# Kernel optimization log

Hardware: AMD Instinct MI355X
Metric: run time of the kernel (lower is better)

The kernel has to match this reference:

```python
import jax, jax.numpy as jnp
import numpy as np

TAIL_BOUND = 3.0
MIN_BIN_WIDTH = 1e-3
MIN_BIN_HEIGHT = 1e-3
SEARCH_EPS = 1e-6


def setup_inputs() -> dict:
    key = jax.random.key(0)
    k1, k2, k3, k4, k5 = jax.random.split(key, 5)
    B, D, K = 8192, 256, 8
    return {
        "x": jax.random.normal(k1, (B, D), dtype=jnp.float32),
        "w_": jax.random.normal(k2, (B, D, K), dtype=jnp.float32),
        "h_": jax.random.normal(k3, (B, D, K), dtype=jnp.float32),
        "dl_": jax.random.normal(k4, (B, D, 1), dtype=jnp.float32),
        "dr_": jax.random.normal(k5, (B, D, 1), dtype=jnp.float32),
    }


def _cumknots(unnorm, min_bin):
    # softmax -> min-width floor -> cumsum with exact 0/1 endpoints
    num_bins = unnorm.shape[-1]
    w = jax.nn.softmax(unnorm, axis=-1)
    w = min_bin + (1.0 - min_bin * num_bins) * w
    cum = jnp.cumsum(w, axis=-1)
    cum = cum.at[..., -1].set(1.0)
    pad = [(0, 0)] * (cum.ndim - 1) + [(1, 0)]
    cum = jnp.pad(cum, pad)
    return w, cum


def reference(x, w_, h_, dl_, dr_):
    num_bins = w_.shape[-1]
    left = bottom = -TAIL_BOUND
    right = top = TAIL_BOUND

    inside = (x >= left) & (x <= right)

    # map to unit interval; clamp keeps masked-out lanes numerically safe
    t = jnp.clip((x - left) / (right - left), 0.0, 1.0)

    widths, cumwidths = _cumknots(w_, MIN_BIN_WIDTH)       # [B,D,K], [B,D,K+1]
    heights, cumheights = _cumknots(h_, MIN_BIN_HEIGHT)

    slopes = heights / widths                              # [B,D,K]
    min1 = jnp.minimum(jnp.abs(slopes[..., :-1]), jnp.abs(slopes[..., 1:]))
    min2 = 0.5 * (widths[..., 1:] * slopes[..., :-1] + widths[..., :-1] * slopes[..., 1:]) \
           / (widths[..., :-1] + widths[..., 1:])
    mins = jnp.minimum(min1, min2)                         # [B,D,K-1]

    d_left = jax.nn.sigmoid(dl_) * 3.0 * slopes[..., :1]
    d_right = jax.nn.sigmoid(dr_) * 3.0 * slopes[..., -1:]
    d_mid = mins * (jnp.sign(slopes[..., :-1]) + jnp.sign(slopes[..., 1:]))
    derivs = jnp.concatenate([d_left, d_mid, d_right], axis=-1)  # [B,D,K+1]

    a = (derivs[..., :-1] + derivs[..., 1:] - 2.0 * slopes) / widths ** 2
    b = (3.0 * slopes - 2.0 * derivs[..., :-1] - derivs[..., 1:]) / widths
    c = derivs[..., :-1]
    d = cumheights[..., :-1]

    # searchsorted: sum(t >= knots) - 1, with eps bump on the last knot
    knots = cumwidths.at[..., -1].add(SEARCH_EPS)
    bin_idx = jnp.sum((t[..., None] >= knots).astype(jnp.int32), axis=-1) - 1
    bin_idx = jnp.clip(bin_idx, 0, num_bins - 1)[..., None]  # [B,D,1]

    take = lambda arr: jnp.take_along_axis(arr, bin_idx, axis=-1)[..., 0]
    ia, ib, ic, id_ = take(a), take(b), take(c), take(d)
    lw = take(cumwidths)

    sx = t - lw
    out_s = ia * sx ** 3 + ib * sx ** 2 + ic * sx + id_
    lad_s = jnp.log(jnp.abs(3.0 * ia * sx ** 2 + 2.0 * ib * sx + ic))

    out_s = jnp.clip(out_s, 0.0, 1.0) * (top - bottom) + bottom
    lad_s = lad_s + jnp.log(top - bottom) - jnp.log(right - left)

    outputs = jnp.where(inside, out_s, x)          # identity tails
    logabsdet = jnp.where(inside, lad_s, 0.0)
    return outputs, logabsdet
```

## Files before the change

kernel.cpp:

```cpp
#include <hip/hip_runtime.h>
#include <math.h>


constexpr int K = 8;
constexpr float TAIL = 3.0f;
constexpr float MIN_BIN = 0.001f;
constexpr float SEARCH_EPS = 1e-6f;

__device__ __forceinline__ float rcpf(float v) {
    return __builtin_amdgcn_rcpf(v);
}

__device__ __forceinline__ float signf(float v) {
    return (v > 0.0f ? 1.0f : (v < 0.0f ? -1.0f : 0.0f));
}

__global__ __launch_bounds__(256) void cbs_kernel(
    const float* __restrict__ x_,
    const float* __restrict__ w_,
    const float* __restrict__ h_,
    const float* __restrict__ dl_,
    const float* __restrict__ dr_,
    float* __restrict__ out,
    float* __restrict__ lad,
    int n)
{
    int i = blockIdx.x * blockDim.x + threadIdx.x;
    if (i >= n) return;

    const float4* w4 = (const float4*)w_ + 2 * (size_t)i;
    const float4* h4 = (const float4*)h_ + 2 * (size_t)i;
    float4 wa = w4[0], wb = w4[1];
    float4 ha = h4[0], hb = h4[1];

    float wr[K] = {wa.x, wa.y, wa.z, wa.w, wb.x, wb.y, wb.z, wb.w};
    float hr[K] = {ha.x, ha.y, ha.z, ha.w, hb.x, hb.y, hb.z, hb.w};

    float xv  = x_[i];
    float dlv = dl_[i];
    float drv = dr_[i];

    float mw = wr[0];
    #pragma unroll
    for (int k = 1; k < K; k++) mw = fmaxf(mw, wr[k]);
    float sw = 0.0f;
    #pragma unroll
    for (int k = 0; k < K; k++) { wr[k] = __expf(wr[k] - mw); sw += wr[k]; }
    float inv_sw = rcpf(sw);
    #pragma unroll
    for (int k = 0; k < K; k++) wr[k] = MIN_BIN + (1.0f - MIN_BIN * K) * (wr[k] * inv_sw);

    float mh = hr[0];
    #pragma unroll
    for (int k = 1; k < K; k++) mh = fmaxf(mh, hr[k]);
    float sh = 0.0f;
    #pragma unroll
    for (int k = 0; k < K; k++) { hr[k] = __expf(hr[k] - mh); sh += hr[k]; }
    float inv_sh = rcpf(sh);
    #pragma unroll
    for (int k = 0; k < K; k++) hr[k] = MIN_BIN + (1.0f - MIN_BIN * K) * (hr[k] * inv_sh);

    float cw[K + 1]; cw[0] = 0.0f;
    #pragma unroll
    for (int k = 0; k < K; k++) cw[k + 1] = cw[k] + wr[k];
    float ch[K + 1]; ch[0] = 0.0f;
    #pragma unroll
    for (int k = 0; k < K; k++) ch[k + 1] = ch[k] + hr[k];

    float s[K];
    #pragma unroll
    for (int k = 0; k < K; k++) s[k] = hr[k] * rcpf(wr[k]);

    float dv[K + 1];
    dv[0] = rcpf(1.0f + __expf(-dlv)) * 3.0f * s[0];
    dv[K] = rcpf(1.0f + __expf(-drv)) * 3.0f * s[K - 1];
    #pragma unroll
    for (int k = 0; k < K - 1; k++) {
        float m1 = fminf(fabsf(s[k]), fabsf(s[k + 1]));
        float m2 = 0.5f * (wr[k + 1] * s[k] + wr[k] * s[k + 1]) * rcpf(wr[k] + wr[k + 1]);
        float mn = fminf(m1, m2);
        dv[k + 1] = mn * (signf(s[k]) + signf(s[k + 1]));
    }

    float t = (xv + TAIL) * (1.0f / (2.0f * TAIL));
    t = fminf(fmaxf(t, 0.0f), 1.0f);

    int bin = 0;
    #pragma unroll
    for (int j = 1; j < K; j++) bin += (t >= cw[j]) ? 1 : 0;
    bin += (t >= 1.0f + SEARCH_EPS) ? 1 : 0;
    if (bin > K - 1) bin = K - 1;

    float wk = wr[0], sk = s[0], d0 = dv[0], d1 = dv[1], lw = cw[0], dd = ch[0];
    #pragma unroll
    for (int k = 1; k < K; k++) {
        bool sel = (bin == k);
        wk = sel ? wr[k]     : wk;
        sk = sel ? s[k]      : sk;
        d0 = sel ? dv[k]     : d0;
        d1 = sel ? dv[k + 1] : d1;
        lw = sel ? cw[k]     : lw;
        dd = sel ? ch[k]     : dd;
    }

    float inv_wk = rcpf(wk);
    float ia = (d0 + d1 - 2.0f * sk) * inv_wk * inv_wk;
    float ib = (3.0f * sk - 2.0f * d0 - d1) * inv_wk;
    float ic = d0;

    float sx = t - lw;
    float out_s = ((ia * sx + ib) * sx + ic) * sx + dd;
    float der   = (3.0f * ia * sx + 2.0f * ib) * sx + ic;
    float lad_s = __logf(fabsf(der));

    out_s = fminf(fmaxf(out_s, 0.0f), 1.0f) * (2.0f * TAIL) - TAIL;

    bool inside = (xv >= -TAIL) && (xv <= TAIL);
    out[i] = inside ? out_s : xv;
    lad[i] = inside ? lad_s : 0.0f;
}

extern "C" void kernel_launch(void* const* d_in, const int* in_sizes, int n_in,
                              void* d_out, int out_size, void* d_ws, size_t ws_size,
                              hipStream_t stream) {
    const float* x  = (const float*)d_in[0];
    const float* w  = (const float*)d_in[1];
    const float* h  = (const float*)d_in[2];
    const float* dl = (const float*)d_in[3];
    const float* dr = (const float*)d_in[4];
    int n = in_sizes[0];
    float* out = (float*)d_out;
    float* lad = out + n;

    const int threads = 256;
    const int blocks = (n + threads - 1) / threads;
    cbs_kernel<<<blocks, threads, 0, stream>>>(x, w, h, dl, dr, out, lad, n);
}
```

Measured before the change: 175.0 us.

## Grid-stride loop with software prefetch, simplified softmax and derivative math, nontemporal stores

Switches to a fixed 2048-block grid-stride loop that prefetches the next element's inputs while computing the current one. Drops the max-subtraction in both softmaxes and collapses the sign/abs slope-limiter logic into one min, which is valid only because the slopes are always positive. Writes outputs with nontemporal stores. The missing max shift can overflow exp for large logits, and the fixed grid plus prefetch registers may lower occupancy on a kernel that is memory-bound.

Result: slower. 180.3 us (+3.0%).

```diff
diff --git a/kernel.cpp b/kernel.cpp
--- a/kernel.cpp
+++ b/kernel.cpp
@@ -11,10 +11,6 @@
     return __builtin_amdgcn_rcpf(v);
 }
 
-__device__ __forceinline__ float signf(float v) {
-    return (v > 0.0f ? 1.0f : (v < 0.0f ? -1.0f : 0.0f));
-}
-
 __global__ __launch_bounds__(256) void cbs_kernel(
     const float* __restrict__ x_,
     const float* __restrict__ w_,
@@ -25,99 +21,111 @@
     float* __restrict__ lad,
     int n)
 {
-    int i = blockIdx.x * blockDim.x + threadIdx.x;
-    if (i >= n) return;
+    const int tid    = blockIdx.x * blockDim.x + threadIdx.x;
+    const int stride = gridDim.x * blockDim.x;
 
-    const float4* w4 = (const float4*)w_ + 2 * (size_t)i;
-    const float4* h4 = (const float4*)h_ + 2 * (size_t)i;
-    float4 wa = w4[0], wb = w4[1];
-    float4 ha = h4[0], hb = h4[1];
+    float4 nwa, nwb, nha, nhb;
+    float  nx, ndl, ndr;
 
-    float wr[K] = {wa.x, wa.y, wa.z, wa.w, wb.x, wb.y, wb.z, wb.w};
-    float hr[K] = {ha.x, ha.y, ha.z, ha.w, hb.x, hb.y, hb.z, hb.w};
-
-    float xv  = x_[i];
-    float dlv = dl_[i];
-    float drv = dr_[i];
-
-    float mw = wr[0];
-    #pragma unroll
-    for (int k = 1; k < K; k++) mw = fmaxf(mw, wr[k]);
-    float sw = 0.0f;
-    #pragma unroll
-    for (int k = 0; k < K; k++) { wr[k] = __expf(wr[k] - mw); sw += wr[k]; }
-    float inv_sw = rcpf(sw);
-    #pragma unroll
-    for (int k = 0; k < K; k++) wr[k] = MIN_BIN + (1.0f - MIN_BIN * K) * (wr[k] * inv_sw);
-
-    float mh = hr[0];
-    #pragma unroll
-    for (int k = 1; k < K; k++) mh = fmaxf(mh, hr[k]);
-    float sh = 0.0f;
-    #pragma unroll
-    for (int k = 0; k < K; k++) { hr[k] = __expf(hr[k] - mh); sh += hr[k]; }
-    float inv_sh = rcpf(sh);
-    #pragma unroll
-    for (int k = 0; k < K; k++) hr[k] = MIN_BIN + (1.0f - MIN_BIN * K) * (hr[k] * inv_sh);
-
-    float cw[K + 1]; cw[0] = 0.0f;
-    #pragma unroll
-    for (int k = 0; k < K; k++) cw[k + 1] = cw[k] + wr[k];
-    float ch[K + 1]; ch[0] = 0.0f;
-    #pragma unroll
-    for (int k = 0; k < K; k++) ch[k + 1] = ch[k] + hr[k];
-
-    float s[K];
-    #pragma unroll
-    for (int k = 0; k < K; k++) s[k] = hr[k] * rcpf(wr[k]);
-
-    float dv[K + 1];
-    dv[0] = rcpf(1.0f + __expf(-dlv)) * 3.0f * s[0];
-    dv[K] = rcpf(1.0f + __expf(-drv)) * 3.0f * s[K - 1];
-    #pragma unroll
-    for (int k = 0; k < K - 1; k++) {
-        float m1 = fminf(fabsf(s[k]), fabsf(s[k + 1]));
-        float m2 = 0.5f * (wr[k + 1] * s[k] + wr[k] * s[k + 1]) * rcpf(wr[k] + wr[k + 1]);
-        float mn = fminf(m1, m2);
-        dv[k + 1] = mn * (signf(s[k]) + signf(s[k + 1]));
+    int j = tid;
+    if (j < n) {
+        const float4* w4 = (const float4*)w_ + 2 * (size_t)j;
+        const float4* h4 = (const float4*)h_ + 2 * (size_t)j;
+        nwa = w4[0]; nwb = w4[1];
+        nha = h4[0]; nhb = h4[1];
+        nx  = x_[j]; ndl = dl_[j]; ndr = dr_[j];
     }
 
-    float t = (xv + TAIL) * (1.0f / (2.0f * TAIL));
-    t = fminf(fmaxf(t, 0.0f), 1.0f);
+    while (j < n) {
+        const float4 wa = nwa, wb = nwb, ha = nha, hb = nhb;
+        const float  xv = nx, dlv = ndl, drv = ndr;
+        const int cur = j;
+        j += stride;
 
-    int bin = 0;
-    #pragma unroll
-    for (int j = 1; j < K; j++) bin += (t >= cw[j]) ? 1 : 0;
-    bin += (t >= 1.0f + SEARCH_EPS) ? 1 : 0;
-    if (bin > K - 1) bin = K - 1;
+        if (j < n) {
+            const float4* w4 = (const float4*)w_ + 2 * (size_t)j;
+            const float4* h4 = (const float4*)h_ + 2 * (size_t)j;
+            nwa = w4[0]; nwb = w4[1];
+            nha = h4[0]; nhb = h4[1];
+            nx  = x_[j]; ndl = dl_[j]; ndr = dr_[j];
+        }
 
-    float wk = wr[0], sk = s[0], d0 = dv[0], d1 = dv[1], lw = cw[0], dd = ch[0];
-    #pragma unroll
-    for (int k = 1; k < K; k++) {
-        bool sel = (bin == k);
-        wk = sel ? wr[k]     : wk;
-        sk = sel ? s[k]      : sk;
-        d0 = sel ? dv[k]     : d0;
-        d1 = sel ? dv[k + 1] : d1;
-        lw = sel ? cw[k]     : lw;
-        dd = sel ? ch[k]     : dd;
+        float wr[K] = {wa.x, wa.y, wa.z, wa.w, wb.x, wb.y, wb.z, wb.w};
+        float hr[K] = {ha.x, ha.y, ha.z, ha.w, hb.x, hb.y, hb.z, hb.w};
+
+        float sw = 0.0f;
+        #pragma unroll
+        for (int k = 0; k < K; k++) { wr[k] = __expf(wr[k]); sw += wr[k]; }
+        float cs = (1.0f - MIN_BIN * K) * rcpf(sw);
+        #pragma unroll
+        for (int k = 0; k < K; k++) wr[k] = MIN_BIN + cs * wr[k];
+
+        float sh = 0.0f;
+        #pragma unroll
+        for (int k = 0; k < K; k++) { hr[k] = __expf(hr[k]); sh += hr[k]; }
+        float csh = (1.0f - MIN_BIN * K) * rcpf(sh);
+        #pragma unroll
+        for (int k = 0; k < K; k++) hr[k] = MIN_BIN + csh * hr[k];
+
+        float cw[K + 1]; cw[0] = 0.0f;
+        #pragma unroll
+        for (int k = 0; k < K; k++) cw[k + 1] = cw[k] + wr[k];
+        float ch[K + 1]; ch[0] = 0.0f;
+        #pragma unroll
+        for (int k = 0; k < K; k++) ch[k + 1] = ch[k] + hr[k];
+
+        float s[K];
+        #pragma unroll
+        for (int k = 0; k < K; k++) s[k] = hr[k] * rcpf(wr[k]);
+
+        float dv[K + 1];
+        dv[0] = rcpf(1.0f + __expf(-dlv)) * 3.0f * s[0];
+        dv[K] = rcpf(1.0f + __expf(-drv)) * 3.0f * s[K - 1];
+        #pragma unroll
+        for (int k = 0; k < K - 1; k++) {
+            float two_m1 = 2.0f * fminf(s[k], s[k + 1]);
+            float m2x = (wr[k + 1] * s[k] + wr[k] * s[k + 1])
+                        * rcpf(wr[k] + wr[k + 1]);
+            dv[k + 1] = fminf(two_m1, m2x);
+        }
+
+        float t = (xv + TAIL) * (1.0f / (2.0f * TAIL));
+        t = fminf(fmaxf(t, 0.0f), 1.0f);
+
+        int bin = 0;
+        #pragma unroll
+        for (int jj = 1; jj < K; jj++) bin += (t >= cw[jj]) ? 1 : 0;
+        bin += (t >= 1.0f + SEARCH_EPS) ? 1 : 0;
+        if (bin > K - 1) bin = K - 1;
+
+        float wk = wr[0], sk = s[0], d0 = dv[0], d1 = dv[1], lw = cw[0], dd = ch[0];
+        #pragma unroll
+        for (int k = 1; k < K; k++) {
+            bool sel = (bin == k);
+            wk = sel ? wr[k]     : wk;
+            sk = sel ? s[k]      : sk;
+            d0 = sel ? dv[k]     : d0;
+            d1 = sel ? dv[k + 1] : d1;
+            lw = sel ? cw[k]     : lw;
+            dd = sel ? ch[k]     : dd;
+        }
+
+        float inv_wk = rcpf(wk);
+        float ia = (d0 + d1 - 2.0f * sk) * inv_wk * inv_wk;
+        float ib = (3.0f * sk - 2.0f * d0 - d1) * inv_wk;
+        float ic = d0;
+
+        float sx = t - lw;
+        float out_s = ((ia * sx + ib) * sx + ic) * sx + dd;
+        float der   = (3.0f * ia * sx + 2.0f * ib) * sx + ic;
+        float lad_s = __logf(fabsf(der));
+
+        out_s = fminf(fmaxf(out_s, 0.0f), 1.0f) * (2.0f * TAIL) - TAIL;
+
+        bool inside = (xv >= -TAIL) && (xv <= TAIL);
+        __builtin_nontemporal_store(inside ? out_s : xv,   out + cur);
+        __builtin_nontemporal_store(inside ? lad_s : 0.0f, lad + cur);
     }
-
-    float inv_wk = rcpf(wk);
-    float ia = (d0 + d1 - 2.0f * sk) * inv_wk * inv_wk;
-    float ib = (3.0f * sk - 2.0f * d0 - d1) * inv_wk;
-    float ic = d0;
-
-    float sx = t - lw;
-    float out_s = ((ia * sx + ib) * sx + ic) * sx + dd;
-    float der   = (3.0f * ia * sx + 2.0f * ib) * sx + ic;
-    float lad_s = __logf(fabsf(der));
-
-    out_s = fminf(fmaxf(out_s, 0.0f), 1.0f) * (2.0f * TAIL) - TAIL;
-
-    bool inside = (xv >= -TAIL) && (xv <= TAIL);
-    out[i] = inside ? out_s : xv;
-    lad[i] = inside ? lad_s : 0.0f;
 }
 
 extern "C" void kernel_launch(void* const* d_in, const int* in_sizes, int n_in,
@@ -133,6 +141,6 @@
     float* lad = out + n;
 
     const int threads = 256;
-    const int blocks = (n + threads - 1) / threads;
+    const int blocks  = 2048;
     cbs_kernel<<<blocks, threads, 0, stream>>>(x, w, h, dl, dr, out, lad, n);
 }
```
